# Kernel tuning notes

Hardware: AMD Instinct MI355X
Metric: run time of the kernel (lower is better)

The kernel has to match this reference:

```python
import jax, jax.numpy as jnp
import numpy as np

CLAMP_MIN = -10.0
CLAMP_MAX = 10.0
B = 8
N = 100_000
EDGES = 3_200_000


def setup_inputs() -> dict:
    key = jax.random.key(0)
    ks = jax.random.split(key, 9)
    chem_influence = jax.random.normal(ks[0], (B, N), dtype=jnp.float32)
    E = jax.random.normal(ks[1], (B, N), dtype=jnp.float32)
    O = jax.random.normal(ks[2], (B, N), dtype=jnp.float32)
    src = jax.random.randint(ks[3], (EDGES,), 0, N, dtype=jnp.int64) if jax.config.jax_enable_x64 else jax.random.randint(ks[3], (EDGES,), 0, N).astype(jnp.int32)
    dst = jax.random.randint(ks[4], (EDGES,), 0, N).astype(src.dtype)
    w = jax.random.normal(ks[5], (EDGES,), dtype=jnp.float32)
    o_pre = jax.random.normal(ks[6], (B, N), dtype=jnp.float32)
    # learned per-neuron params (rnd_init=True ranges from the module)
    threshold = jax.random.uniform(ks[7], (N,), minval=-1.0, maxval=2.0, dtype=jnp.float32)
    decay = jax.random.uniform(ks[8], (N,), minval=0.05, maxval=1.0, dtype=jnp.float32)
    return {"chem_influence": chem_influence, "E": E, "O": O, "src": src,
            "dst": dst, "w": w, "o_pre": o_pre, "threshold": threshold, "decay": decay}


def reference(chem_influence, E, O, src, dst, w, o_pre, threshold, decay):
    # Gap-junction path: gather presyn output Oj and postsyn internal state En per edge
    Oj = o_pre[:, src]                    # (B, E)
    En = E[:, dst]                        # (B, E)
    contrib = Oj * w * jnp.sign(Oj - En)  # sign(Oj - En) * w_j * Oj
    # scatter-add edge contributions into the chemical-influence buffer (dup indices accumulate)
    chem = chem_influence.at[:, dst].add(contrib)  # (B, N)
    # Neuron dynamics (eqs 10, 11)
    S = jnp.clip(E + chem, CLAMP_MIN, CLAMP_MAX)
    gt = S > threshold
    mask = (~gt) & (S == E)
    new_o = jax.nn.relu(S - threshold)
    new_e = jnp.where(gt, new_o, jnp.where(mask, E - decay, S))
    # torch module returns (new_o, (new_e, new_o)); flatten the state tuple
    return new_o, new_e
```

## Files before the change

### kernel.cpp

```cpp
#include <hip/hip_runtime.h>

#define CLAMP_MIN_F (-10.0f)
#define CLAMP_MAX_F (10.0f)
#define BATCH 8
#define R_LOG 5
#define RNODES 32
#define ASTR 9
#define EPB 16384
#define TB_BIN 1024
#define MAX4K 4096
#define SCHUNK 2048
#define MAXH (SCHUNK / 256)

__global__ void prep_o_kernel(const float* __restrict__ o_pre,
                              float* __restrict__ o_preT,
                              unsigned* __restrict__ total,
                              int N) {
    int n = blockIdx.x * blockDim.x + threadIdx.x;
    if (n < MAX4K) total[n] = 0u;
    if (n >= N) return;
    float o[BATCH];
    #pragma unroll
    for (int b = 0; b < BATCH; ++b) o[b] = o_pre[b * N + n];
    float4* op = (float4*)&o_preT[(size_t)n * BATCH];
    op[0] = make_float4(o[0], o[1], o[2], o[3]);
    op[1] = make_float4(o[4], o[5], o[6], o[7]);
}

__global__ void hist_reserve_kernel(const int* __restrict__ dst,
                                    unsigned* __restrict__ total,
                                    unsigned* __restrict__ offs0,
                                    int edges, int KPAD) {
    __shared__ unsigned sh[MAX4K];
    int bid = blockIdx.x;
    for (int k = threadIdx.x; k < KPAD; k += blockDim.x) sh[k] = 0u;
    __syncthreads();
    int start = bid * EPB;
    int end = min(edges, start + EPB);
    for (int i = start + threadIdx.x; i < end; i += blockDim.x)
        atomicAdd(&sh[((unsigned)dst[i]) >> R_LOG], 1u);
    __syncthreads();
    for (int k = threadIdx.x; k < KPAD; k += blockDim.x) {
        unsigned c = sh[k];
        offs0[(size_t)bid * KPAD + k] = c ? atomicAdd(&total[k], c) : 0u;
    }
}

__global__ void scan4_kernel(const unsigned* __restrict__ total,
                             unsigned* __restrict__ base,
                             int KPAD) {
    __shared__ unsigned s1[1024];
    __shared__ unsigned s2[1024];
    int t = threadIdx.x;
    unsigned v0 = (4 * t     < KPAD) ? total[4 * t]     : 0u;
    unsigned v1 = (4 * t + 1 < KPAD) ? total[4 * t + 1] : 0u;
    unsigned v2 = (4 * t + 2 < KPAD) ? total[4 * t + 2] : 0u;
    unsigned v3 = (4 * t + 3 < KPAD) ? total[4 * t + 3] : 0u;
    unsigned sum = v0 + v1 + v2 + v3;
    s1[t] = sum;
    __syncthreads();
    unsigned* cur = s1;
    unsigned* nxt = s2;
    for (int off = 1; off < 1024; off <<= 1) {
        unsigned x = cur[t];
        if (t >= off) x += cur[t - off];
        nxt[t] = x;
        __syncthreads();
        unsigned* tmp = cur; cur = nxt; nxt = tmp;
    }
    unsigned incl = cur[t];
    unsigned excl = incl - sum;
    base[4 * t]     = excl;
    base[4 * t + 1] = excl + v0;
    base[4 * t + 2] = excl + v0 + v1;
    base[4 * t + 3] = excl + v0 + v1 + v2;
    if (t == 1023) base[4096] = incl;
}

__global__ void scatter_kernel(const int* __restrict__ src,
                               const int* __restrict__ dst,
                               const float* __restrict__ w,
                               const unsigned* __restrict__ offs0,
                               const unsigned* __restrict__ base,
                               int2* __restrict__ recS,
                               int edges, int KPAD) {
    __shared__ unsigned loffs[MAX4K];
    int bid = blockIdx.x;
    for (int k = threadIdx.x; k < KPAD; k += blockDim.x)
        loffs[k] = base[k] + offs0[(size_t)bid * KPAD + k];
    __syncthreads();
    int start = bid * EPB;
    int end = min(edges, start + EPB);
    for (int i = start + threadIdx.x; i < end; i += blockDim.x) {
        int d = dst[i];
        int s = src[i];
        float wv = w[i];
        unsigned k = ((unsigned)d) >> R_LOG;
        unsigned pos = atomicAdd(&loffs[k], 1u);
        unsigned key = (((unsigned)d & (RNODES - 1)) << 26) | (unsigned)s;
        recS[pos] = make_int2((int)key, __float_as_int(wv));
    }
}

__global__ __launch_bounds__(256)
void accum_kernel(const int2* __restrict__ recS,
                  const unsigned* __restrict__ base,
                  const float* __restrict__ o_preT,
                  const float* __restrict__ E,
                  const float* __restrict__ chem_in,
                  const float* __restrict__ thr,
                  const float* __restrict__ decay,
                  float* __restrict__ new_o,
                  float* __restrict__ new_e,
                  int N) {
    __shared__ int2 srec[SCHUNK];
    __shared__ float e_lds[RNODES * ASTR];
    __shared__ float acc_st[RNODES * ASTR];
    __shared__ unsigned cnt[RNODES];
    __shared__ unsigned sstart[RNODES + 1];
    int k = blockIdx.x;
    int ns = k << R_LOG;
    int cnt_n = min(RNODES, N - ns);
    int tid = threadIdx.x;

    for (int i = tid; i < RNODES * BATCH; i += blockDim.x) {
        int b = i >> R_LOG;
        int n = i & (RNODES - 1);
        if (n < cnt_n) e_lds[n * ASTR + b] = E[(size_t)b * N + ns + n];
    }
    __syncthreads();

    int b = tid & 7;
    int g = tid >> 3;
    float En = e_lds[g * ASTR + b];
    float accv = 0.f;

    unsigned b0 = base[k], b1 = base[k + 1];
    for (unsigned cs = b0; cs < b1; cs += SCHUNK) {
        unsigned m = min((unsigned)SCHUNK, b1 - cs);
        if (tid < RNODES) cnt[tid] = 0u;
        __syncthreads();

        int2 hrec[MAXH];
        unsigned hmeta[MAXH];
        #pragma unroll
        for (int j = 0; j < MAXH; ++j) {
            unsigned i = (unsigned)tid + (unsigned)j * blockDim.x;
            if (i < m) {
                int2 rec = recS[cs + i];
                unsigned dl = ((unsigned)rec.x >> 26) & (RNODES - 1);
                unsigned pos = atomicAdd(&cnt[dl], 1u);
                hrec[j] = rec;
                hmeta[j] = (dl << 16) | pos;
            } else {
                hmeta[j] = 0xFFFFFFFFu;
            }
        }
        __syncthreads();
        if (tid == 0) {
            unsigned run = 0;
            for (int d = 0; d < RNODES; ++d) { sstart[d] = run; run += cnt[d]; }
            sstart[RNODES] = run;
        }
        __syncthreads();
        #pragma unroll
        for (int j = 0; j < MAXH; ++j) {
            if (hmeta[j] != 0xFFFFFFFFu) {
                unsigned dl = hmeta[j] >> 16;
                unsigned pos = hmeta[j] & 0xFFFFu;
                srec[sstart[dl] + pos] = hrec[j];
            }
        }
        __syncthreads();

        unsigned st = sstart[g];
        unsigned en = st + cnt[g];
        for (unsigned r = st; r < en; ++r) {
            int2 rec = srec[r];
            unsigned s = (unsigned)rec.x & 0x3FFFFFFu;
            float Oj = o_preT[((size_t)s << 3) + b];
            float wv = __int_as_float(rec.y);
            float df = Oj - En;
            float sg = (df > 0.f) ? 1.f : ((df < 0.f) ? -1.f : 0.f);
            accv += Oj * wv * sg;
        }
        __syncthreads();
    }

    acc_st[g * ASTR + b] = accv;
    __syncthreads();

    for (int i = tid; i < RNODES * BATCH; i += blockDim.x) {
        int bb = i >> R_LOG;
        int n = i & (RNODES - 1);
        if (n >= cnt_n) continue;
        float e = e_lds[n * ASTR + bb];
        float S = e + chem_in[(size_t)bb * N + ns + n] + acc_st[n * ASTR + bb];
        S = fminf(fmaxf(S, CLAMP_MIN_F), CLAMP_MAX_F);
        float t  = thr[ns + n];
        float dc = decay[ns + n];
        bool gt = S > t;
        float no = fmaxf(S - t, 0.f);
        float ne = gt ? no : ((S == e) ? (e - dc) : S);
        new_o[(size_t)bb * N + ns + n] = no;
        new_e[(size_t)bb * N + ns + n] = ne;
    }
}

__global__ void prep_kernel(const float* __restrict__ chem_in,
                            const float* __restrict__ o_pre,
                            const float* __restrict__ E,
                            float* __restrict__ chemT,
                            float* __restrict__ o_preT,
                            float* __restrict__ E_T,
                            int N) {
    int n = blockIdx.x * blockDim.x + threadIdx.x;
    if (n >= N) return;
    float c[BATCH], o[BATCH], ee[BATCH];
    #pragma unroll
    for (int b = 0; b < BATCH; ++b) {
        c[b]  = chem_in[b * N + n];
        o[b]  = o_pre[b * N + n];
        ee[b] = E[b * N + n];
    }
    float4* cp = (float4*)&chemT[(size_t)n * BATCH];
    cp[0] = make_float4(c[0], c[1], c[2], c[3]);
    cp[1] = make_float4(c[4], c[5], c[6], c[7]);
    float4* op = (float4*)&o_preT[(size_t)n * BATCH];
    op[0] = make_float4(o[0], o[1], o[2], o[3]);
    op[1] = make_float4(o[4], o[5], o[6], o[7]);
    float4* ep = (float4*)&E_T[(size_t)n * BATCH];
    ep[0] = make_float4(ee[0], ee[1], ee[2], ee[3]);
    ep[1] = make_float4(ee[4], ee[5], ee[6], ee[7]);
}
__global__ void edge_scatter_eb(const int* __restrict__ src,
                                const int* __restrict__ dst,
                                const float* __restrict__ w,
                                const float* __restrict__ o_preT,
                                const float* __restrict__ E_T,
                                float* __restrict__ chemT,
                                int edges) {
    int t = blockIdx.x * blockDim.x + threadIdx.x;
    int e = t >> 3;
    int b = t & 7;
    if (e >= edges) return;
    int s = src[e]; int d = dst[e]; float we = w[e];
    float Oj = o_preT[(size_t)s * BATCH + b];
    float En = E_T[(size_t)d * BATCH + b];
    float diff = Oj - En;
    float sg = (diff > 0.0f) ? 1.0f : ((diff < 0.0f) ? -1.0f : 0.0f);
    atomicAdd(&chemT[(size_t)d * BATCH + b], Oj * we * sg);
}
__global__ void finalize_nb(const float* __restrict__ E,
                            const float* __restrict__ chemT,
                            const float* __restrict__ thr,
                            const float* __restrict__ decay,
                            float* __restrict__ new_o,
                            float* __restrict__ new_e, int N) {
    int n = blockIdx.x * blockDim.x + threadIdx.x;
    if (n >= N) return;
    const float4* cp = (const float4*)&chemT[(size_t)n * BATCH];
    float4 c0 = cp[0], c1 = cp[1];
    float c[BATCH] = {c0.x, c0.y, c0.z, c0.w, c1.x, c1.y, c1.z, c1.w};
    float t = thr[n];
    float dc = decay[n];
    #pragma unroll
    for (int b = 0; b < BATCH; ++b) {
        int i = b * N + n;
        float e = E[i];
        float S = fminf(fmaxf(e + c[b], CLAMP_MIN_F), CLAMP_MAX_F);
        bool gt = S > t;
        float no = fmaxf(S - t, 0.0f);
        float ne = gt ? no : ((S == e) ? (e - dc) : S);
        new_o[i] = no;
        new_e[i] = ne;
    }
}

static inline size_t align256(size_t x) { return (x + 255) & ~(size_t)255; }

extern "C" void kernel_launch(void* const* d_in, const int* in_sizes, int n_in,
                              void* d_out, int out_size, void* d_ws, size_t ws_size,
                              hipStream_t stream) {
    const float* chem_influence = (const float*)d_in[0];
    const float* E              = (const float*)d_in[1];
    const int*   src            = (const int*)d_in[3];
    const int*   dst            = (const int*)d_in[4];
    const float* w              = (const float*)d_in[5];
    const float* o_pre          = (const float*)d_in[6];
    const float* threshold      = (const float*)d_in[7];
    const float* decay          = (const float*)d_in[8];

    const int edges = in_sizes[3];
    const int BN    = in_sizes[0];
    const int N     = in_sizes[7];

    float* new_o = (float*)d_out;
    float* new_e = (float*)d_out + BN;

    const int TB = 256;
    int nblk = (N + TB - 1) / TB;

    const int K    = (N + RNODES - 1) >> R_LOG;
    const int KPAD = (K + 63) & ~63;
    const int NB   = (edges + EPB - 1) / EPB;

    size_t off = 0;
    size_t opreT_off  = off; off += align256((size_t)BN * 4);
    size_t base_off   = off; off += align256((size_t)(MAX4K + 1) * 4);
    size_t total_off  = off; off += align256((size_t)MAX4K * 4);
    size_t offs0_off  = off; off += align256((size_t)NB * KPAD * 4);
    size_t rec_off    = off; off += align256((size_t)edges * 8);
    size_t need = off;

    char* wsb = (char*)d_ws;

    if (K <= MAX4K - 1 && ws_size >= need) {
        float*    o_preT = (float*)(wsb + opreT_off);
        unsigned* base   = (unsigned*)(wsb + base_off);
        unsigned* total  = (unsigned*)(wsb + total_off);
        unsigned* offs0  = (unsigned*)(wsb + offs0_off);
        int2*     recS   = (int2*)(wsb + rec_off);

        prep_o_kernel<<<nblk, TB, 0, stream>>>(o_pre, o_preT, total, N);
        hist_reserve_kernel<<<NB, TB_BIN, 0, stream>>>(dst, total, offs0, edges, KPAD);
        scan4_kernel<<<1, 1024, 0, stream>>>(total, base, KPAD);
        scatter_kernel<<<NB, TB_BIN, 0, stream>>>(src, dst, w, offs0, base, recS, edges, KPAD);
        accum_kernel<<<K, TB, 0, stream>>>(recS, base, o_preT, E,
                                           chem_influence, threshold, decay,
                                           new_o, new_e, N);
    } else if (ws_size >= 3 * (size_t)BN * 4) {
        float* chemT  = (float*)d_ws;
        float* o_preT = chemT + BN;
        float* E_T    = o_preT + BN;
        prep_kernel<<<nblk, TB, 0, stream>>>(chem_influence, o_pre, E,
                                             chemT, o_preT, E_T, N);
        long long ethreads = (long long)edges * BATCH;
        int gblk = (int)((ethreads + TB - 1) / TB);
        edge_scatter_eb<<<gblk, TB, 0, stream>>>(src, dst, w, o_preT, E_T,
                                                 chemT, edges);
        finalize_nb<<<nblk, TB, 0, stream>>>(E, chemT, threshold, decay,
                                             new_o, new_e, N);
    }
}
```

Before: 92.43 us.

## Bin edges into 256-node super-buckets with LDS-staged coalesced scatter

Edge bucketing moves from 32-node buckets to 256-node super-buckets: the histogram and global scan now cover at most 512 bins. The scatter kernel locally sorts each 2048-edge chunk by bucket in LDS and writes records to global memory in contiguous runs instead of one random write per edge. The accumulate kernel runs 1024 threads per super-bucket and handles two node groups per thread. It also adds a barrier to the scan to remove a read/write race, and limits the fast path to N up to 2^17 because the source index is now packed into 17 bits. Larger buckets mean fewer blocks and fewer atomic-reserved bins, at the cost of more per-chunk LDS scan barriers.

```diff
diff --git a/kernel.cpp b/kernel.cpp
--- a/kernel.cpp
+++ b/kernel.cpp
@@ -3,14 +3,14 @@
 #define CLAMP_MIN_F (-10.0f)
 #define CLAMP_MAX_F (10.0f)
 #define BATCH 8
-#define R_LOG 5
-#define RNODES 32
-#define ASTR 9
+#define SUP_LOG 8
+#define SNODES 256
+#define MAXS 512
+#define ESTR 9
 #define EPB 16384
+#define CH 2048
 #define TB_BIN 1024
 #define MAX4K 4096
-#define SCHUNK 2048
-#define MAXH (SCHUNK / 256)
 
 __global__ void prep_o_kernel(const float* __restrict__ o_pre,
                               float* __restrict__ o_preT,
@@ -27,22 +27,23 @@
     op[1] = make_float4(o[4], o[5], o[6], o[7]);
 }
 
-__global__ void hist_reserve_kernel(const int* __restrict__ dst,
-                                    unsigned* __restrict__ total,
-                                    unsigned* __restrict__ offs0,
-                                    int edges, int KPAD) {
-    __shared__ unsigned sh[MAX4K];
-    int bid = blockIdx.x;
-    for (int k = threadIdx.x; k < KPAD; k += blockDim.x) sh[k] = 0u;
+__global__ __launch_bounds__(TB_BIN)
+void hist_reserve_kernel(const int* __restrict__ dst,
+                         unsigned* __restrict__ superTotal,
+                         unsigned* __restrict__ offs0s,
+                         int edges) {
+    __shared__ unsigned sh[MAXS];
+    int bid = blockIdx.x, tid = threadIdx.x;
+    for (int s = tid; s < MAXS; s += blockDim.x) sh[s] = 0u;
     __syncthreads();
     int start = bid * EPB;
-    int end = min(edges, start + EPB);
-    for (int i = start + threadIdx.x; i < end; i += blockDim.x)
-        atomicAdd(&sh[((unsigned)dst[i]) >> R_LOG], 1u);
+    int endE = min(edges, start + EPB);
+    for (int i = start + tid; i < endE; i += blockDim.x)
+        atomicAdd(&sh[((unsigned)dst[i]) >> SUP_LOG], 1u);
     __syncthreads();
-    for (int k = threadIdx.x; k < KPAD; k += blockDim.x) {
-        unsigned c = sh[k];
-        offs0[(size_t)bid * KPAD + k] = c ? atomicAdd(&total[k], c) : 0u;
+    for (int s = tid; s < MAXS; s += blockDim.x) {
+        unsigned c = sh[s];
+        offs0s[(size_t)bid * MAXS + s] = c ? atomicAdd(&superTotal[s], c) : 0u;
     }
 }
 
@@ -64,6 +65,7 @@
     for (int off = 1; off < 1024; off <<= 1) {
         unsigned x = cur[t];
         if (t >= off) x += cur[t - off];
+        __syncthreads();
         nxt[t] = x;
         __syncthreads();
         unsigned* tmp = cur; cur = nxt; nxt = tmp;
@@ -74,37 +76,91 @@
     base[4 * t + 1] = excl + v0;
     base[4 * t + 2] = excl + v0 + v1;
     base[4 * t + 3] = excl + v0 + v1 + v2;
-    if (t == 1023) base[4096] = incl;
-}
-
-__global__ void scatter_kernel(const int* __restrict__ src,
-                               const int* __restrict__ dst,
-                               const float* __restrict__ w,
-                               const unsigned* __restrict__ offs0,
-                               const unsigned* __restrict__ base,
-                               int2* __restrict__ recS,
-                               int edges, int KPAD) {
-    __shared__ unsigned loffs[MAX4K];
-    int bid = blockIdx.x;
-    for (int k = threadIdx.x; k < KPAD; k += blockDim.x)
-        loffs[k] = base[k] + offs0[(size_t)bid * KPAD + k];
-    __syncthreads();
+    if (t == 1023) base[MAX4K] = incl;
+}
+
+__global__ __launch_bounds__(TB_BIN)
+void scatter_kernel(const int* __restrict__ src,
+                    const int* __restrict__ dst,
+                    const float* __restrict__ w,
+                    const unsigned* __restrict__ offs0s,
+                    const unsigned* __restrict__ baseS,
+                    int2* __restrict__ recS,
+                    int edges) {
+    __shared__ int2 srec[CH];
+    __shared__ unsigned short ssup[CH];
+    __shared__ unsigned cnt[MAXS];
+    __shared__ unsigned sstart[MAXS];
+    __shared__ unsigned cursor[MAXS];
+    __shared__ unsigned pa[MAXS];
+    __shared__ unsigned pb[MAXS];
+    int bid = blockIdx.x, tid = threadIdx.x;
+    for (int s = tid; s < MAXS; s += blockDim.x)
+        cursor[s] = baseS[s] + offs0s[(size_t)bid * MAXS + s];
     int start = bid * EPB;
-    int end = min(edges, start + EPB);
-    for (int i = start + threadIdx.x; i < end; i += blockDim.x) {
-        int d = dst[i];
-        int s = src[i];
-        float wv = w[i];
-        unsigned k = ((unsigned)d) >> R_LOG;
-        unsigned pos = atomicAdd(&loffs[k], 1u);
-        unsigned key = (((unsigned)d & (RNODES - 1)) << 26) | (unsigned)s;
-        recS[pos] = make_int2((int)key, __float_as_int(wv));
-    }
-}
-
-__global__ __launch_bounds__(256)
+    int endE = min(edges, start + EPB);
+    for (int cs = start; cs < endE; cs += CH) {
+        int m = min(CH, endE - cs);
+        __syncthreads();
+        for (int s = tid; s < MAXS; s += blockDim.x) cnt[s] = 0u;
+        __syncthreads();
+        int2 hrec[2]; unsigned hsup[2], hpos[2]; bool hv[2];
+        #pragma unroll
+        for (int j = 0; j < 2; ++j) {
+            int i = tid + j * TB_BIN;
+            hv[j] = (i < m);
+            if (hv[j]) {
+                int gi = cs + i;
+                int d = dst[gi];
+                unsigned key = (((unsigned)d & (SNODES - 1)) << 17) | (unsigned)src[gi];
+                hrec[j] = make_int2((int)key, __float_as_int(w[gi]));
+                hsup[j] = (unsigned)d >> SUP_LOG;
+                hpos[j] = atomicAdd(&cnt[hsup[j]], 1u);
+            }
+        }
+        __syncthreads();
+        {
+            unsigned* cur = pa;
+            unsigned* nxt = pb;
+            if (tid < MAXS) cur[tid] = cnt[tid];
+            __syncthreads();
+            for (int off = 1; off < MAXS; off <<= 1) {
+                unsigned v = 0;
+                if (tid < MAXS) { v = cur[tid]; if (tid >= off) v += cur[tid - off]; }
+                __syncthreads();
+                if (tid < MAXS) nxt[tid] = v;
+                __syncthreads();
+                unsigned* t2 = cur; cur = nxt; nxt = t2;
+            }
+            if (tid < MAXS) sstart[tid] = cur[tid] - cnt[tid];
+            __syncthreads();
+        }
+        #pragma unroll
+        for (int j = 0; j < 2; ++j) {
+            if (hv[j]) {
+                unsigned idx = sstart[hsup[j]] + hpos[j];
+                srec[idx] = hrec[j];
+                ssup[idx] = (unsigned short)hsup[j];
+            }
+        }
+        __syncthreads();
+        #pragma unroll
+        for (int j = 0; j < 2; ++j) {
+            int i = tid + j * TB_BIN;
+            if (i < m) {
+                unsigned sup = ssup[i];
+                unsigned gpos = cursor[sup] + ((unsigned)i - sstart[sup]);
+                recS[gpos] = srec[i];
+            }
+        }
+        __syncthreads();
+        for (int s = tid; s < MAXS; s += blockDim.x) cursor[s] += cnt[s];
+    }
+}
+
+__global__ __launch_bounds__(TB_BIN)
 void accum_kernel(const int2* __restrict__ recS,
-                  const unsigned* __restrict__ base,
+                  const unsigned* __restrict__ baseS,
                   const float* __restrict__ o_preT,
                   const float* __restrict__ E,
                   const float* __restrict__ chem_in,
@@ -113,89 +169,107 @@
                   float* __restrict__ new_o,
                   float* __restrict__ new_e,
                   int N) {
-    __shared__ int2 srec[SCHUNK];
-    __shared__ float e_lds[RNODES * ASTR];
-    __shared__ float acc_st[RNODES * ASTR];
-    __shared__ unsigned cnt[RNODES];
-    __shared__ unsigned sstart[RNODES + 1];
-    int k = blockIdx.x;
-    int ns = k << R_LOG;
-    int cnt_n = min(RNODES, N - ns);
+    __shared__ int2 srec[CH];
+    __shared__ float e_lds[SNODES * ESTR];
+    __shared__ float acc_st[SNODES * ESTR];
+    __shared__ unsigned cnt[SNODES];
+    __shared__ unsigned sstart[SNODES];
+    __shared__ unsigned pa[SNODES];
+    __shared__ unsigned pb[SNODES];
+    int sb = blockIdx.x;
+    int ns = sb << SUP_LOG;
+    int cntn = min(SNODES, N - ns);
     int tid = threadIdx.x;
 
-    for (int i = tid; i < RNODES * BATCH; i += blockDim.x) {
-        int b = i >> R_LOG;
-        int n = i & (RNODES - 1);
-        if (n < cnt_n) e_lds[n * ASTR + b] = E[(size_t)b * N + ns + n];
+    for (int i = tid; i < SNODES * BATCH; i += blockDim.x) {
+        int b = i >> SUP_LOG;
+        int n = i & (SNODES - 1);
+        if (n < cntn) e_lds[n * ESTR + b] = E[(size_t)b * N + ns + n];
     }
     __syncthreads();
 
     int b = tid & 7;
     int g = tid >> 3;
-    float En = e_lds[g * ASTR + b];
-    float accv = 0.f;
-
-    unsigned b0 = base[k], b1 = base[k + 1];
-    for (unsigned cs = b0; cs < b1; cs += SCHUNK) {
-        unsigned m = min((unsigned)SCHUNK, b1 - cs);
-        if (tid < RNODES) cnt[tid] = 0u;
-        __syncthreads();
-
-        int2 hrec[MAXH];
-        unsigned hmeta[MAXH];
+    float En0 = e_lds[g * ESTR + b];
+    float En1 = e_lds[(g + 128) * ESTR + b];
+    float acc0 = 0.f, acc1 = 0.f;
+
+    unsigned r0 = baseS[sb], r1 = baseS[sb + 1];
+    for (unsigned cs = r0; cs < r1; cs += CH) {
+        unsigned m = min((unsigned)CH, r1 - cs);
+        for (int s = tid; s < SNODES; s += blockDim.x) cnt[s] = 0u;
+        __syncthreads();
+        int2 hrec[2]; unsigned hdl[2], hpos[2]; bool hv[2];
         #pragma unroll
-        for (int j = 0; j < MAXH; ++j) {
-            unsigned i = (unsigned)tid + (unsigned)j * blockDim.x;
-            if (i < m) {
+        for (int j = 0; j < 2; ++j) {
+            unsigned i = (unsigned)tid + (unsigned)j * TB_BIN;
+            hv[j] = (i < m);
+            if (hv[j]) {
                 int2 rec = recS[cs + i];
-                unsigned dl = ((unsigned)rec.x >> 26) & (RNODES - 1);
-                unsigned pos = atomicAdd(&cnt[dl], 1u);
+                unsigned dl = ((unsigned)rec.x >> 17) & (SNODES - 1);
                 hrec[j] = rec;
-                hmeta[j] = (dl << 16) | pos;
-            } else {
-                hmeta[j] = 0xFFFFFFFFu;
-            }
-        }
-        __syncthreads();
-        if (tid == 0) {
-            unsigned run = 0;
-            for (int d = 0; d < RNODES; ++d) { sstart[d] = run; run += cnt[d]; }
-            sstart[RNODES] = run;
-        }
-        __syncthreads();
+                hdl[j] = dl;
+                hpos[j] = atomicAdd(&cnt[dl], 1u);
+            }
+        }
+        __syncthreads();
+        {
+            unsigned* cur = pa;
+            unsigned* nxt = pb;
+            if (tid < SNODES) cur[tid] = cnt[tid];
+            __syncthreads();
+            for (int off = 1; off < SNODES; off <<= 1) {
+                unsigned v = 0;
+                if (tid < SNODES) { v = cur[tid]; if (tid >= off) v += cur[tid - off]; }
+                __syncthreads();
+                if (tid < SNODES) nxt[tid] = v;
+                __syncthreads();
+                unsigned* t2 = cur; cur = nxt; nxt = t2;
+            }
+            if (tid < SNODES) sstart[tid] = cur[tid] - cnt[tid];
+            __syncthreads();
+        }
         #pragma unroll
-        for (int j = 0; j < MAXH; ++j) {
-            if (hmeta[j] != 0xFFFFFFFFu) {
-                unsigned dl = hmeta[j] >> 16;
-                unsigned pos = hmeta[j] & 0xFFFFu;
-                srec[sstart[dl] + pos] = hrec[j];
-            }
-        }
-        __syncthreads();
-
-        unsigned st = sstart[g];
-        unsigned en = st + cnt[g];
-        for (unsigned r = st; r < en; ++r) {
-            int2 rec = srec[r];
-            unsigned s = (unsigned)rec.x & 0x3FFFFFFu;
-            float Oj = o_preT[((size_t)s << 3) + b];
-            float wv = __int_as_float(rec.y);
-            float df = Oj - En;
-            float sg = (df > 0.f) ? 1.f : ((df < 0.f) ? -1.f : 0.f);
-            accv += Oj * wv * sg;
-        }
-        __syncthreads();
-    }
-
-    acc_st[g * ASTR + b] = accv;
+        for (int j = 0; j < 2; ++j)
+            if (hv[j]) srec[sstart[hdl[j]] + hpos[j]] = hrec[j];
+        __syncthreads();
+        {
+            unsigned st = sstart[g], en = st + cnt[g];
+            for (unsigned r = st; r < en; ++r) {
+                int2 rec = srec[r];
+                unsigned si = (unsigned)rec.x & 0x1FFFFu;
+                float Oj = o_preT[((size_t)si << 3) + b];
+                float wv = __int_as_float(rec.y);
+                float df = Oj - En0;
+                float sg = (df > 0.f) ? 1.f : ((df < 0.f) ? -1.f : 0.f);
+                acc0 += Oj * wv * sg;
+            }
+        }
+        {
+            unsigned st = sstart[g + 128], en = st + cnt[g + 128];
+            for (unsigned r = st; r < en; ++r) {
+                int2 rec = srec[r];
+                unsigned si = (unsigned)rec.x & 0x1FFFFu;
+                float Oj = o_preT[((size_t)si << 3) + b];
+                float wv = __int_as_float(rec.y);
+                float df = Oj - En1;
+                float sg = (df > 0.f) ? 1.f : ((df < 0.f) ? -1.f : 0.f);
+                acc1 += Oj * wv * sg;
+            }
+        }
+        __syncthreads();
+    }
+
+    acc_st[g * ESTR + b] = acc0;
+    acc_st[(g + 128) * ESTR + b] = acc1;
     __syncthreads();
 
-    for (int i = tid; i < RNODES * BATCH; i += blockDim.x) {
-        int bb = i >> R_LOG;
-        int n = i & (RNODES - 1);
-        if (n >= cnt_n) continue;
-        float e = e_lds[n * ASTR + bb];
-        float S = e + chem_in[(size_t)bb * N + ns + n] + acc_st[n * ASTR + bb];
+    for (int i = tid; i < SNODES * BATCH; i += blockDim.x) {
+        int bb = i >> SUP_LOG;
+        int n = i & (SNODES - 1);
+        if (n >= cntn) continue;
+        float e = e_lds[n * ESTR + bb];
+        float S = e + chem_in[(size_t)bb * N + ns + n] + acc_st[n * ESTR + bb];
         S = fminf(fmaxf(S, CLAMP_MIN_F), CLAMP_MAX_F);
         float t  = thr[ns + n];
         float dc = decay[ns + n];
@@ -301,34 +375,34 @@
     const int TB = 256;
     int nblk = (N + TB - 1) / TB;
 
-    const int K    = (N + RNODES - 1) >> R_LOG;
-    const int KPAD = (K + 63) & ~63;
-    const int NB   = (edges + EPB - 1) / EPB;
+    const int NS = (N + SNODES - 1) >> SUP_LOG;
+    const int NB = (edges + EPB - 1) / EPB;
 
     size_t off = 0;
     size_t opreT_off  = off; off += align256((size_t)BN * 4);
     size_t base_off   = off; off += align256((size_t)(MAX4K + 1) * 4);
     size_t total_off  = off; off += align256((size_t)MAX4K * 4);
-    size_t offs0_off  = off; off += align256((size_t)NB * KPAD * 4);
+    size_t offs0_off  = off; off += align256((size_t)NB * MAXS * 4);
     size_t rec_off    = off; off += align256((size_t)edges * 8);
     size_t need = off;
 
     char* wsb = (char*)d_ws;
 
-    if (K <= MAX4K - 1 && ws_size >= need) {
+    if (NS <= MAXS && N <= (1 << 17) && ws_size >= need) {
         float*    o_preT = (float*)(wsb + opreT_off);
-        unsigned* base   = (unsigned*)(wsb + base_off);
+        unsigned* baseS  = (unsigned*)(wsb + base_off);
         unsigned* total  = (unsigned*)(wsb + total_off);
-        unsigned* offs0  = (unsigned*)(wsb + offs0_off);
+        unsigned* offs0s = (unsigned*)(wsb + offs0_off);
         int2*     recS   = (int2*)(wsb + rec_off);
 
         prep_o_kernel<<<nblk, TB, 0, stream>>>(o_pre, o_preT, total, N);
-        hist_reserve_kernel<<<NB, TB_BIN, 0, stream>>>(dst, total, offs0, edges, KPAD);
-        scan4_kernel<<<1, 1024, 0, stream>>>(total, base, KPAD);
-        scatter_kernel<<<NB, TB_BIN, 0, stream>>>(src, dst, w, offs0, base, recS, edges, KPAD);
-        accum_kernel<<<K, TB, 0, stream>>>(recS, base, o_preT, E,
-                                           chem_influence, threshold, decay,
-                                           new_o, new_e, N);
+        hist_reserve_kernel<<<NB, TB_BIN, 0, stream>>>(dst, total, offs0s, edges);
+        scan4_kernel<<<1, 1024, 0, stream>>>(total, baseS, MAXS);
+        scatter_kernel<<<NB, TB_BIN, 0, stream>>>(src, dst, w, offs0s, baseS,
+                                                  recS, edges);
+        accum_kernel<<<NS, TB_BIN, 0, stream>>>(recS, baseS, o_preT, E,
+                                                chem_influence, threshold, decay,
+                                                new_o, new_e, N);
     } else if (ws_size >= 3 * (size_t)BN * 4) {
         float* chemT  = (float*)d_ws;
         float* o_preT = chemT + BN;
```

New measurement: 96.37 us. 4.3% more time.
